# Performance work log

Measured on AMD Instinct MI355X. Metric: run time of the kernel, lower is better.

Reference implementation:

```python
import jax, jax.numpy as jnp
import numpy as np

B, V, C_IN, C_OUT = 4, 8, 32, 32
H, W = 256, 256
G = H * W
K_NEIGHBORS = 3


def compute_adjacency_tilde(extrinsics, k):
    Bv, Vv = extrinsics.shape[:2]
    R = extrinsics[:, :, :3, :3]
    t = extrinsics[:, :, :3, 3]
    # camera centers: -R^T t
    centers = -jnp.einsum('bvji,bvj->bvi', R, t)                 # (B,V,3)
    diff = centers[:, :, None, :] - centers[:, None, :, :]
    dist_sq = jnp.sum(diff * diff, axis=-1)                      # (B,V,V)
    eye = jnp.eye(Vv, dtype=bool)
    sim = jnp.where(eye, -jnp.inf, -dist_sq)
    A_overlap = 1.0 / (1.0 + jnp.sqrt(dist_sq + 1e-6))
    if 0 < k < Vv:
        _, topk_idx = jax.lax.top_k(sim, k)                      # (B,V,k)
        mask = jnp.sum(jax.nn.one_hot(topk_idx, Vv, dtype=jnp.float32), axis=-2) > 0
        A = A_overlap * mask.astype(A_overlap.dtype)
    else:
        A = A_overlap
    A = jnp.where(eye, 1.0, A)                                   # diagonal = 1
    deg = jnp.sum(A, axis=-1, keepdims=True)
    A_tilde = A / (deg + (deg == 0).astype(deg.dtype))
    return A, A_tilde


def setup_inputs() -> dict:
    key = jax.random.key(0)
    k1, k2, k3, k4, k5 = jax.random.split(key, 5)
    features = jax.random.normal(k1, (B, V, G, C_IN), dtype=jnp.float32)
    # projected pixel coords in [0, W-1] x [0, H-1]
    uv = jax.random.uniform(k2, (B, V, V, G, 2), dtype=jnp.float32)
    xy_coords = uv * jnp.array([W - 1, H - 1], dtype=jnp.float32)
    extrinsics = jax.random.normal(k3, (B, V, 4, 4), dtype=jnp.float32)
    W_lin = jax.random.normal(k4, (C_IN, C_OUT), dtype=jnp.float32) * 0.1
    b_lin = jax.random.normal(k5, (C_OUT,), dtype=jnp.float32) * 0.01
    return {"features": features, "xy_coords": xy_coords, "extrinsics": extrinsics,
            "W_lin": W_lin, "b_lin": b_lin}


def reference(features, xy_coords, extrinsics, W_lin, b_lin):
    feats = features @ W_lin + b_lin                              # (B,V,G,D)
    Bv, Vv, Gv, D = feats.shape
    HW = H * W
    A, A_tilde = compute_adjacency_tilde(extrinsics, K_NEIGHBORS)
    # flattened pixel indices per (batch, src view, tgt view, gaussian)
    x = jnp.clip(jnp.round(xy_coords[..., 0]), 0, W - 1).astype(jnp.int32)
    y = jnp.clip(jnp.round(xy_coords[..., 1]), 0, H - 1).astype(jnp.int32)
    idx = y * W + x                                               # (B,Vsrc,Vtgt,G)
    batch_off = jnp.arange(Bv, dtype=jnp.int32)[:, None] * HW
    outs = []
    for i in range(Vv):  # small fixed number of target views
        w_i = A_tilde[:, i][:, :, None, None]                     # (B,Vsrc,1,1)
        data = (feats * w_i).reshape(Bv * Vv * Gv, D)
        seg = (idx[:, :, i].reshape(Bv, Vv * Gv) + batch_off).reshape(-1)
        grid = jax.ops.segment_sum(data, seg, num_segments=Bv * HW)
        grid = grid.reshape(Bv, HW, D)                            # (B,HW,D)
        self_idx = idx[:, i, i]                                   # (B,G)
        outs.append(jnp.take_along_axis(grid, self_idx[..., None], axis=1))
    stacked = jnp.stack(outs, axis=1)                             # (B,V,G,D)
    return stacked, A
```

## Files before the change

kernel.cpp:

```cpp
#include <hip/hip_runtime.h>
#include <math.h>

#define NB 4
#define NV 8
#define NC 32
#define NG 65536
#define IMGW 256
#define NBI 32
#define RSPLIT 8
#define RBINS (NG / RSPLIT)
#define K4SPLIT 32
#define K4BINS (NG / K4SPLIT)
#define K4CAP 24576
#define CAP4A 1272
#define PART_STRIDE 19456
#define START_STRIDE 65544
#define SORT_STRIDE (1u << 20)
#define SENTINEL (8u << 27)

static constexpr long long STACKED_ELEMS = (long long)NB * NV * NG * NC;

typedef __attribute__((ext_vector_type(8))) short short8;
typedef __attribute__((ext_vector_type(4))) float f32x4;
typedef __attribute__((ext_vector_type(4))) unsigned int u32x4;
typedef __attribute__((ext_vector_type(4))) float f32x4c;

static constexpr size_t OFF_AT    = 0;
static constexpr size_t OFF_RTOT  = 1024;
static constexpr size_t OFF_GSC   = 3584;
static constexpr size_t OFF_START = 8192;
static constexpr size_t OFF_CNT   = OFF_START + (size_t)NBI * START_STRIDE * 4;
static constexpr size_t OFF_PIX   = OFF_CNT + (size_t)NBI * NG * 4;
static constexpr size_t OFF_SORT  = OFF_PIX + (size_t)NBI * NV * NG * 2;
static constexpr size_t OFF_FB16  = OFF_SORT + (size_t)NBI * SORT_STRIDE * 4;
static constexpr size_t OFF_PARTS = OFF_FB16;

__device__ __forceinline__ unsigned short f2bf(float f)
{
    unsigned int u = __float_as_uint(f);
    return (unsigned short)((u + 0x7FFFu + ((u >> 16) & 1u)) >> 16);
}

__global__ __launch_bounds__(256) void k1_pix(const float2* __restrict__ xy,
                                              unsigned short* __restrict__ pixarr,
                                              const float* __restrict__ ext,
                                              float* __restrict__ A_out,
                                              float* __restrict__ At_out)
{
    if (blockIdx.x == 16384) {
        __shared__ float ctr[NB * NV][3];
        __shared__ float Dsh[NB * NV * NV];
        int t = threadIdx.x;
        if (t < NB * NV) {
            const float* E = ext + t * 16;
            #pragma unroll
            for (int i = 0; i < 3; i++) {
                float s = E[0 * 4 + i] * E[0 * 4 + 3]
                        + E[1 * 4 + i] * E[1 * 4 + 3]
                        + E[2 * 4 + i] * E[2 * 4 + 3];
                ctr[t][i] = -s;
            }
        }
        __syncthreads();
        {
            int b = t >> 6, i = (t >> 3) & 7, j = t & 7;
            float dx = ctr[b * 8 + i][0] - ctr[b * 8 + j][0];
            float dy = ctr[b * 8 + i][1] - ctr[b * 8 + j][1];
            float dz = ctr[b * 8 + i][2] - ctr[b * 8 + j][2];
            Dsh[t] = dx * dx + dy * dy + dz * dz;
        }
        __syncthreads();
        if (t < NB * NV) {
            int ri = t & 7;
            const float* drow = &Dsh[t * 8];
            bool chosen[8] = {false, false, false, false, false, false, false, false};
            for (int n = 0; n < 3; n++) {
                int best = -1; float bs = -3.0e38f;
                for (int j2 = 0; j2 < 8; j2++) {
                    if (j2 == ri || chosen[j2]) continue;
                    float s = -drow[j2];
                    if (s > bs) { bs = s; best = j2; }
                }
                chosen[best] = true;
            }
            float row[8]; float deg = 0.f;
            #pragma unroll
            for (int j2 = 0; j2 < 8; j2++) {
                float a = 0.f;
                if (j2 == ri)        a = 1.0f;
                else if (chosen[j2]) a = 1.0f / (1.0f + sqrtf(drow[j2] + 1e-6f));
                row[j2] = a; deg += a;
            }
            float dn = deg + (deg == 0.f ? 1.f : 0.f);
            #pragma unroll
            for (int j2 = 0; j2 < 8; j2++) {
                A_out[t * 8 + j2]  = row[j2];
                At_out[t * 8 + j2] = row[j2] / dn;
            }
        }
        return;
    }
    unsigned int base = blockIdx.x * 1024 + threadIdx.x;
    #pragma unroll
    for (int k = 0; k < 4; k++) {
        unsigned int tid = base + k * 256;
        float2 p = xy[tid];
        float px = fminf(fmaxf(rintf(p.x), 0.f), (float)(IMGW - 1));
        float py = fminf(fmaxf(rintf(p.y), 0.f), (float)(IMGW - 1));
        unsigned int pix = (unsigned int)py * IMGW + (unsigned int)px;
        unsigned int g = tid & 0xFFFFu;
        unsigned int i = (tid >> 16) & 7u;
        unsigned int j = (tid >> 19) & 7u;
        unsigned int b = tid >> 22;
        unsigned int bi = (b << 3) | i;
        pixarr[(((bi << 3) | j) << 16) | g] = (unsigned short)pix;
    }
}

__global__ __launch_bounds__(1024) void k2_hist(const unsigned short* __restrict__ pixarr,
                                                unsigned int* __restrict__ cnt,
                                                unsigned int* __restrict__ rtot)
{
    __shared__ unsigned int hist[RBINS];
    int t = threadIdx.x;
    unsigned int bi = blockIdx.x & 31u;
    unsigned int r  = blockIdx.x >> 5;
    unsigned int r0 = r * RBINS;
    for (int k = t; k < RBINS; k += 1024) hist[k] = 0;
    __syncthreads();
    const uint4* src = (const uint4*)(pixarr + ((size_t)bi << 19));
    for (int it = 0; it < 8; it++) {
        uint4 vv[8];
        #pragma unroll
        for (int q = 0; q < 8; q++)
            vv[q] = src[t + (it * 8 + q) * 1024];
        #pragma unroll
        for (int q = 0; q < 8; q++) {
            const unsigned int* vw = (const unsigned int*)&vv[q];
            #pragma unroll
            for (int h = 0; h < 4; h++) {
                unsigned int w = vw[h];
                unsigned int p0 = (w & 0xFFFFu) - r0;
                unsigned int p1 = (w >> 16) - r0;
                if (p0 < RBINS) atomicAdd(&hist[p0], 1u);
                if (p1 < RBINS) atomicAdd(&hist[p1], 1u);
            }
        }
    }
    __syncthreads();
    unsigned int* dst = cnt + ((size_t)bi << 16) + r0;
    unsigned int psum = 0;
    for (int k = t; k < RBINS; k += 1024) {
        unsigned int v = hist[k];
        dst[k] = v;
        psum += (v + 7u) & ~7u;
    }
    __syncthreads();
    hist[t] = psum;
    __syncthreads();
    for (int off = 512; off; off >>= 1) {
        if (t < off) hist[t] += hist[t + off];
        __syncthreads();
    }
    if (t == 0) rtot[bi * 8 + r] = hist[0];
}

__global__ __launch_bounds__(1024) void k3c_scan(const unsigned int* __restrict__ cnt,
                                                 const unsigned int* __restrict__ rtot,
                                                 unsigned int* __restrict__ start)
{
    __shared__ unsigned int lc[RBINS];
    __shared__ unsigned int bs[1024];
    int t = threadIdx.x;
    unsigned int bi = blockIdx.x & 31u;
    unsigned int r  = blockIdx.x >> 5;
    unsigned int r0 = r * RBINS;
    unsigned int rb = 0, rtotal = 0;
    #pragma unroll
    for (int q = 0; q < 8; q++) {
        unsigned int v = rtot[bi * 8 + q];
        if ((unsigned int)q < r) rb += v;
        rtotal += v;
    }
    const unsigned int* c = cnt + ((size_t)bi << 16) + r0;
    #pragma unroll
    for (int q = 0; q < 8; q++)
        lc[q * 1024 + t] = (c[q * 1024 + t] + 7u) & ~7u;
    __syncthreads();
    unsigned int v[8]; unsigned int s = 0;
    #pragma unroll
    for (int k = 0; k < 8; k++) { v[k] = s; s += lc[t * 8 + k]; }
    bs[t] = s;
    __syncthreads();
    for (int off = 1; off < 1024; off <<= 1) {
        unsigned int u = (t >= off) ? bs[t - off] : 0u;
        __syncthreads();
        bs[t] += u;
        __syncthreads();
    }
    unsigned int base = rb + bs[t] - s;
    #pragma unroll
    for (int k = 0; k < 8; k++) lc[t * 8 + k] = base + v[k];
    __syncthreads();
    unsigned int* st_ = start + (size_t)bi * START_STRIDE + r0;
    #pragma unroll
    for (int q = 0; q < 8; q++)
        st_[q * 1024 + t] = lc[q * 1024 + t];
    if (r == 7 && t == 0)
        start[(size_t)bi * START_STRIDE + NG] = rtotal;
}

__global__ __launch_bounds__(1024) void k4a_part(const unsigned short* __restrict__ pixarr,
                                                 unsigned int* __restrict__ gsc,
                                                 unsigned int* __restrict__ parts)
{
    extern __shared__ unsigned int dynA[];
    unsigned int* cur32 = dynA;
    unsigned int* res   = dynA + 32;
    unsigned int* lcnt  = dynA + 64;
    unsigned int* lbuck = dynA + 96;
    int t = threadIdx.x;
    unsigned int bi    = blockIdx.x & 31u;
    unsigned int chunk = blockIdx.x >> 5;
    if (t < 32) cur32[t] = 0;
    __syncthreads();
    const uint4* src = (const uint4*)(pixarr + ((size_t)bi << 19)) + (chunk << 12);
    unsigned int idx0 = chunk << 15;
    #pragma unroll
    for (int it = 0; it < 4; it++) {
        uint4 v = src[t + it * 1024];
        unsigned int base_idx = idx0 + (t + it * 1024) * 8;
        const unsigned int* vw = (const unsigned int*)&v;
        #pragma unroll
        for (int h = 0; h < 8; h++) {
            unsigned int pix = (h & 1) ? (vw[h >> 1] >> 16) : (vw[h >> 1] & 0xFFFFu);
            unsigned int sub = pix >> 11;
            unsigned int pv = ((pix & 0x7FFu) << 19) | (base_idx + h);
            unsigned int slot = atomicAdd(&cur32[sub], 1u);
            if (slot < CAP4A) {
                lbuck[sub * CAP4A + slot] = pv;
            } else {
                unsigned int gs = atomicAdd(&gsc[(bi << 5) | sub], 1u);
                parts[(size_t)((bi << 5) | sub) * PART_STRIDE + gs] = pv;
            }
        }
    }
    __syncthreads();
    if (t < 32) {
        unsigned int n = cur32[t];
        n = n < CAP4A ? n : CAP4A;
        lcnt[t] = n;
        res[t] = atomicAdd(&gsc[(bi << 5) | t], n);
    }
    __syncthreads();
    for (int s = 0; s < 32; s++) {
        unsigned int n = lcnt[s];
        unsigned int b0 = res[s];
        unsigned int* dst = parts + (size_t)((bi << 5) | s) * PART_STRIDE + b0;
        const unsigned int* sb = lbuck + s * CAP4A;
        for (unsigned int k = t; k < n; k += 1024) dst[k] = sb[k];
    }
}

__global__ __launch_bounds__(1024) void k4b_fill(const unsigned int* __restrict__ gsc,
                                                 const unsigned int* __restrict__ parts,
                                                 const unsigned int* __restrict__ start,
                                                 unsigned int* __restrict__ sorted)
{
    extern __shared__ unsigned int dynB[];
    unsigned int* cur = dynB;
    unsigned int* buf = dynB + K4BINS;
    int t = threadIdx.x;
    unsigned int bi  = blockIdx.x & 31u;
    unsigned int sub = blockIdx.x >> 5;
    unsigned int bin0 = sub * K4BINS;
    const unsigned int* stg = start + (size_t)bi * START_STRIDE;
    unsigned int base = stg[bin0];
    unsigned int end  = stg[bin0 + K4BINS];
    unsigned int size = end - base;
    unsigned int n = gsc[(bi << 5) | sub];
    const unsigned int* seg = parts + (size_t)((bi << 5) | sub) * PART_STRIDE;
    unsigned int* dstbase = sorted + (size_t)bi * SORT_STRIDE;

    if (size <= K4CAP) {
        #pragma unroll 2
        for (int k = t; k < K4BINS; k += 1024) cur[k] = stg[bin0 + k] - base;
        for (int k = t; k < (int)size; k += 1024) buf[k] = SENTINEL;
        __syncthreads();
        for (unsigned int k = t; k < n; k += 1024) {
            unsigned int pv = seg[k];
            unsigned int bin = pv >> 19;
            unsigned int slot = atomicAdd(&cur[bin], 1u);
            buf[slot] = (((pv >> 16) & 7u) << 27) | ((pv & 0x7FFFFu) << 6);
        }
        __syncthreads();
        uint4* gdst = (uint4*)(dstbase + base);
        const uint4* lsrc = (const uint4*)buf;
        int n4 = (int)(size >> 2);
        for (int k = t; k < n4; k += 1024) gdst[k] = lsrc[k];
    } else {
        #pragma unroll 2
        for (int k = t; k < K4BINS; k += 1024) cur[k] = stg[bin0 + k];
        __syncthreads();
        for (unsigned int k = t; k < n; k += 1024) {
            unsigned int pv = seg[k];
            unsigned int bin = pv >> 19;
            unsigned int slot = atomicAdd(&cur[bin], 1u);
            dstbase[slot] = (((pv >> 16) & 7u) << 27) | ((pv & 0x7FFFFu) << 6);
        }
        __syncthreads();
        for (int k = t; k < K4BINS; k += 1024) {
            unsigned int e = stg[bin0 + k + 1];
            for (unsigned int x = cur[k]; x < e; x++) dstbase[x] = SENTINEL;
        }
    }
}

__global__ __launch_bounds__(256) void kf_conv(const float* __restrict__ src,
                                               ushort4* __restrict__ dst)
{
    unsigned int base = blockIdx.x * 1024 + threadIdx.x;
    #pragma unroll
    for (int k = 0; k < 4; k++) {
        unsigned int idx = base + k * 256;
        f32x4c v = __builtin_nontemporal_load((const f32x4c*)(src) + idx);
        ushort4 o;
        o.x = f2bf(v.x); o.y = f2bf(v.y); o.z = f2bf(v.z); o.w = f2bf(v.w);
        dst[idx] = o;
    }
}

__global__ __launch_bounds__(256, 4) void b_gather(
    const unsigned short* __restrict__ fb16,
    const unsigned short* __restrict__ pixarr,
    const unsigned int* __restrict__ start,
    const unsigned int* __restrict__ sorted,
    const float* __restrict__ Wlin,
    const float* __restrict__ blin,
    const float* __restrict__ At,
    float* __restrict__ out,
    int b)
{
    __shared__ float At9[NBI][16];
    int t = threadIdx.x;
    int c4 = t & 7;
    int grp = t >> 3;

    unsigned int bidx = blockIdx.x;
    unsigned int i  = bidx & 7u;
    unsigned int gc = bidx >> 3;
    unsigned int bi = ((unsigned int)b << 3) | i;
    unsigned int g0 = gc << 5;
    unsigned int g = g0 + grp;

    unsigned int pix = pixarr[(((bi << 3) | i) << 16) | g];
    const unsigned int* st = start + (size_t)bi * START_STRIDE;
    unsigned int s0 = st[pix];
    unsigned int e0 = st[pix + 1];
    const unsigned int* pl = sorted + (size_t)bi * SORT_STRIDE;
    u32x4 pa = __builtin_nontemporal_load((const u32x4*)(pl + s0));
    u32x4 pb = __builtin_nontemporal_load((const u32x4*)(pl + s0 + 4));

    At9[t >> 3][t & 7] = At[t];
    At9[t >> 3][8 + (t & 7)] = 0.f;
    int l = t & 63;
    short8 bf0, bf1;
    #pragma unroll
    for (int j = 0; j < 8; j++) {
        int kk = (l >> 4) * 8 + j;
        bf0[j] = (short)f2bf(Wlin[kk * NC + (l & 15)]);
        bf1[j] = (short)f2bf(Wlin[kk * NC + 16 + (l & 15)]);
    }
    const char* fbB = (const char*)fb16;
    unsigned int cb = c4 << 3;
    __syncthreads();

    const float* Atrow = At9[bi];
    float ax = 0.f, ay = 0.f, az = 0.f, aw = 0.f, wsum = 0.f;
    for (unsigned int k0 = s0; k0 < e0; k0 += 8) {
        unsigned int pv[8] = {pa.x, pa.y, pa.z, pa.w, pb.x, pb.y, pb.z, pb.w};
        uint2 uv[8];
        #pragma unroll
        for (int h = 0; h < 8; h++)
            uv[h] = *(const uint2*)(fbB + ((pv[h] & 0x01FFFFC0u) | cb));
        if (k0 + 8 < e0) {
            pa = __builtin_nontemporal_load((const u32x4*)(pl + k0 + 8));
            pb = __builtin_nontemporal_load((const u32x4*)(pl + k0 + 12));
        }
        float wv[8];
        #pragma unroll
        for (int h = 0; h < 8; h++)
            wv[h] = Atrow[pv[h] >> 27];
        #pragma unroll
        for (int h = 0; h < 8; h++) {
            ax = fmaf(wv[h], __uint_as_float(uv[h].x << 16), ax);
            ay = fmaf(wv[h], __uint_as_float(uv[h].x & 0xFFFF0000u), ay);
            az = fmaf(wv[h], __uint_as_float(uv[h].y << 16), az);
            aw = fmaf(wv[h], __uint_as_float(uv[h].y & 0xFFFF0000u), aw);
            wsum += wv[h];
        }
    }

    int r = l & 15;
    int kb = l >> 4;
    int s0l = (((r & 7) << 3) | (kb << 1)) & 63;
    int s1l = s0l | 1;
    float v0x = __shfl(ax, s0l, 64), v0y = __shfl(ay, s0l, 64);
    float v0z = __shfl(az, s0l, 64), v0w = __shfl(aw, s0l, 64);
    float v1x = __shfl(ax, s1l, 64), v1y = __shfl(ay, s1l, 64);
    float v1z = __shfl(az, s1l, 64), v1w = __shfl(aw, s1l, 64);
    short8 af;
    if (r < 8) {
        af[0] = (short)f2bf(v0x); af[1] = (short)f2bf(v0y);
        af[2] = (short)f2bf(v0z); af[3] = (short)f2bf(v0w);
        af[4] = (short)f2bf(v1x); af[5] = (short)f2bf(v1y);
        af[6] = (short)f2bf(v1z); af[7] = (short)f2bf(v1w);
    } else {
        af = short8{0, 0, 0, 0, 0, 0, 0, 0};
    }
    float bias0 = blin[l & 15];
    float bias1 = blin[16 + (l & 15)];
    f32x4 c0, c1;
    #pragma unroll
    for (int q = 0; q < 4; q++) {
        int row = kb * 4 + q;
        float wvx = __shfl(wsum, (row << 3) & 63, 64);
        wvx = (row < 8) ? wvx : 0.f;
        c0[q] = bias0 * wvx;
        c1[q] = bias1 * wvx;
    }
    c0 = __builtin_amdgcn_mfma_f32_16x16x32_bf16(af, bf0, c0, 0, 0, 0);
    c1 = __builtin_amdgcn_mfma_f32_16x16x32_bf16(af, bf1, c1, 0, 0, 0);
    if (l < 32) {
        size_t rowbase = (((size_t)bi << 16) | g0) + (t >> 6) * 8;
        #pragma unroll
        for (int q = 0; q < 4; q++) {
            size_t rr = rowbase + (l >> 4) * 4 + q;
            __builtin_nontemporal_store(c0[q], &out[rr * NC + (l & 15)]);
            __builtin_nontemporal_store(c1[q], &out[rr * NC + 16 + (l & 15)]);
        }
    }
}

extern "C" void kernel_launch(void* const* d_in, const int* in_sizes, int n_in,
                              void* d_out, int out_size, void* d_ws, size_t ws_size,
                              hipStream_t stream)
{
    const float* features = (const float*)d_in[0];
    const float* xy       = (const float*)d_in[1];
    const float* ext      = (const float*)d_in[2];
    const float* Wlin     = (const float*)d_in[3];
    const float* blin     = (const float*)d_in[4];
    float* out = (float*)d_out;

    char* ws = (char*)d_ws;
    float*          At     = (float*)(ws + OFF_AT);
    unsigned int*   rtot   = (unsigned int*)(ws + OFF_RTOT);
    unsigned int*   gsc    = (unsigned int*)(ws + OFF_GSC);
    unsigned int*   start  = (unsigned int*)(ws + OFF_START);
    unsigned int*   cnt    = (unsigned int*)(ws + OFF_CNT);
    unsigned short* pixarr = (unsigned short*)(ws + OFF_PIX);
    unsigned int*   sorted = (unsigned int*)(ws + OFF_SORT);
    unsigned int*   parts  = (unsigned int*)(ws + OFF_PARTS);
    unsigned short* fb16   = (unsigned short*)(ws + OFF_FB16);

    static const size_t k4a_lds = (96 + 32 * CAP4A) * sizeof(unsigned int);
    static const size_t k4b_lds = (K4BINS + K4CAP) * sizeof(unsigned int);
    hipFuncSetAttribute((const void*)k4a_part,
                        hipFuncAttributeMaxDynamicSharedMemorySize, (int)k4a_lds);
    hipFuncSetAttribute((const void*)k4b_fill,
                        hipFuncAttributeMaxDynamicSharedMemorySize, (int)k4b_lds);

    k1_pix<<<16385, 256, 0, stream>>>((const float2*)xy, pixarr, ext,
                                      out + STACKED_ELEMS, At);
    k2_hist<<<NBI * RSPLIT, 1024, 0, stream>>>(pixarr, cnt, rtot);
    k3c_scan<<<NBI * RSPLIT, 1024, 0, stream>>>(cnt, rtot, start);

    hipMemsetAsync(gsc, 0, 1024 * sizeof(unsigned int), stream);
    k4a_part<<<NBI * 16, 1024, k4a_lds, stream>>>(pixarr, gsc, parts);
    k4b_fill<<<NBI * K4SPLIT, 1024, k4b_lds, stream>>>(gsc, parts, start, sorted);

    for (int b = 0; b < NB; b++) {
        const float* src = features + (((size_t)b) << 19) * NC;
        kf_conv<<<4096, 256, 0, stream>>>(src, (ushort4*)fb16);
        b_gather<<<16384, 256, 0, stream>>>(fb16, pixarr, start, sorted,
                                            Wlin, blin, At, out, b);
    }
}
```

Before: 592.1 us.

## Derive bin offsets from partitioned buckets instead of a full histogram pass

Drops the separate histogram and scan kernels that each re-read the whole pixel-index array. Per-bucket histograms and local prefix sums are now computed from the already partitioned bucket data, followed by a tiny cross-bucket scan. The fill kernel writes the global start offsets itself. This removes one full pass over the pixel array, at the cost of two extra small launches and a per-bucket local-start buffer.

```diff
diff --git a/kernel.cpp b/kernel.cpp
--- a/kernel.cpp
+++ b/kernel.cpp
@@ -7,8 +7,6 @@
 #define NG 65536
 #define IMGW 256
 #define NBI 32
-#define RSPLIT 8
-#define RBINS (NG / RSPLIT)
 #define K4SPLIT 32
 #define K4BINS (NG / K4SPLIT)
 #define K4CAP 24576
@@ -25,15 +23,16 @@
 typedef __attribute__((ext_vector_type(4))) unsigned int u32x4;
 typedef __attribute__((ext_vector_type(4))) float f32x4c;
 
-static constexpr size_t OFF_AT    = 0;
-static constexpr size_t OFF_RTOT  = 1024;
-static constexpr size_t OFF_GSC   = 3584;
-static constexpr size_t OFF_START = 8192;
-static constexpr size_t OFF_CNT   = OFF_START + (size_t)NBI * START_STRIDE * 4;
-static constexpr size_t OFF_PIX   = OFF_CNT + (size_t)NBI * NG * 4;
-static constexpr size_t OFF_SORT  = OFF_PIX + (size_t)NBI * NV * NG * 2;
-static constexpr size_t OFF_FB16  = OFF_SORT + (size_t)NBI * SORT_STRIDE * 4;
-static constexpr size_t OFF_PARTS = OFF_FB16;
+static constexpr size_t OFF_AT     = 0;
+static constexpr size_t OFF_PTOT   = 1024;
+static constexpr size_t OFF_PBASE  = 5120;
+static constexpr size_t OFF_GSC    = 9216;
+static constexpr size_t OFF_START  = 16384;
+static constexpr size_t OFF_LSTART = OFF_START + (size_t)NBI * START_STRIDE * 4;
+static constexpr size_t OFF_PIX    = OFF_LSTART + (size_t)1024 * K4BINS * 4;
+static constexpr size_t OFF_SORT   = OFF_PIX + (size_t)NBI * NV * NG * 2;
+static constexpr size_t OFF_FB16   = OFF_SORT + (size_t)NBI * SORT_STRIDE * 4;
+static constexpr size_t OFF_PARTS  = OFF_FB16;
 
 __device__ __forceinline__ unsigned short f2bf(float f)
 {
@@ -117,99 +116,6 @@
     }
 }
 
-__global__ __launch_bounds__(1024) void k2_hist(const unsigned short* __restrict__ pixarr,
-                                                unsigned int* __restrict__ cnt,
-                                                unsigned int* __restrict__ rtot)
-{
-    __shared__ unsigned int hist[RBINS];
-    int t = threadIdx.x;
-    unsigned int bi = blockIdx.x & 31u;
-    unsigned int r  = blockIdx.x >> 5;
-    unsigned int r0 = r * RBINS;
-    for (int k = t; k < RBINS; k += 1024) hist[k] = 0;
-    __syncthreads();
-    const uint4* src = (const uint4*)(pixarr + ((size_t)bi << 19));
-    for (int it = 0; it < 8; it++) {
-        uint4 vv[8];
-        #pragma unroll
-        for (int q = 0; q < 8; q++)
-            vv[q] = src[t + (it * 8 + q) * 1024];
-        #pragma unroll
-        for (int q = 0; q < 8; q++) {
-            const unsigned int* vw = (const unsigned int*)&vv[q];
-            #pragma unroll
-            for (int h = 0; h < 4; h++) {
-                unsigned int w = vw[h];
-                unsigned int p0 = (w & 0xFFFFu) - r0;
-                unsigned int p1 = (w >> 16) - r0;
-                if (p0 < RBINS) atomicAdd(&hist[p0], 1u);
-                if (p1 < RBINS) atomicAdd(&hist[p1], 1u);
-            }
-        }
-    }
-    __syncthreads();
-    unsigned int* dst = cnt + ((size_t)bi << 16) + r0;
-    unsigned int psum = 0;
-    for (int k = t; k < RBINS; k += 1024) {
-        unsigned int v = hist[k];
-        dst[k] = v;
-        psum += (v + 7u) & ~7u;
-    }
-    __syncthreads();
-    hist[t] = psum;
-    __syncthreads();
-    for (int off = 512; off; off >>= 1) {
-        if (t < off) hist[t] += hist[t + off];
-        __syncthreads();
-    }
-    if (t == 0) rtot[bi * 8 + r] = hist[0];
-}
-
-__global__ __launch_bounds__(1024) void k3c_scan(const unsigned int* __restrict__ cnt,
-                                                 const unsigned int* __restrict__ rtot,
-                                                 unsigned int* __restrict__ start)
-{
-    __shared__ unsigned int lc[RBINS];
-    __shared__ unsigned int bs[1024];
-    int t = threadIdx.x;
-    unsigned int bi = blockIdx.x & 31u;
-    unsigned int r  = blockIdx.x >> 5;
-    unsigned int r0 = r * RBINS;
-    unsigned int rb = 0, rtotal = 0;
-    #pragma unroll
-    for (int q = 0; q < 8; q++) {
-        unsigned int v = rtot[bi * 8 + q];
-        if ((unsigned int)q < r) rb += v;
-        rtotal += v;
-    }
-    const unsigned int* c = cnt + ((size_t)bi << 16) + r0;
-    #pragma unroll
-    for (int q = 0; q < 8; q++)
-        lc[q * 1024 + t] = (c[q * 1024 + t] + 7u) & ~7u;
-    __syncthreads();
-    unsigned int v[8]; unsigned int s = 0;
-    #pragma unroll
-    for (int k = 0; k < 8; k++) { v[k] = s; s += lc[t * 8 + k]; }
-    bs[t] = s;
-    __syncthreads();
-    for (int off = 1; off < 1024; off <<= 1) {
-        unsigned int u = (t >= off) ? bs[t - off] : 0u;
-        __syncthreads();
-        bs[t] += u;
-        __syncthreads();
-    }
-    unsigned int base = rb + bs[t] - s;
-    #pragma unroll
-    for (int k = 0; k < 8; k++) lc[t * 8 + k] = base + v[k];
-    __syncthreads();
-    unsigned int* st_ = start + (size_t)bi * START_STRIDE + r0;
-    #pragma unroll
-    for (int q = 0; q < 8; q++)
-        st_[q * 1024 + t] = lc[q * 1024 + t];
-    if (r == 7 && t == 0)
-        start[(size_t)bi * START_STRIDE + NG] = rtotal;
-}
-
 __global__ __launch_bounds__(1024) void k4a_part(const unsigned short* __restrict__ pixarr,
                                                  unsigned int* __restrict__ gsc,
                                                  unsigned int* __restrict__ parts)
@@ -262,10 +168,67 @@
     }
 }
 
-__global__ __launch_bounds__(1024) void k4b_fill(const unsigned int* __restrict__ gsc,
+__global__ __launch_bounds__(1024) void k4h_hist(const unsigned int* __restrict__ gsc,
                                                  const unsigned int* __restrict__ parts,
-                                                 const unsigned int* __restrict__ start,
-                                                 unsigned int* __restrict__ sorted)
+                                                 unsigned int* __restrict__ lstart,
+                                                 unsigned int* __restrict__ ptot)
+{
+    __shared__ unsigned int hist[K4BINS];
+    __shared__ unsigned int bs[1024];
+    int t = threadIdx.x;
+    unsigned int bi  = blockIdx.x & 31u;
+    unsigned int sub = blockIdx.x >> 5;
+    unsigned int n = gsc[(bi << 5) | sub];
+    const unsigned int* seg = parts + (size_t)((bi << 5) | sub) * PART_STRIDE;
+    hist[t] = 0; hist[t + 1024] = 0;
+    __syncthreads();
+    for (unsigned int k = t; k < n; k += 1024)
+        atomicAdd(&hist[seg[k] >> 19], 1u);
+    __syncthreads();
+    unsigned int c0 = (hist[2 * t] + 7u) & ~7u;
+    unsigned int c1 = (hist[2 * t + 1] + 7u) & ~7u;
+    unsigned int s = c0 + c1;
+    bs[t] = s;
+    __syncthreads();
+    for (int off = 1; off < 1024; off <<= 1) {
+        unsigned int u = (t >= off) ? bs[t - off] : 0u;
+        __syncthreads();
+        bs[t] += u;
+        __syncthreads();
+    }
+    unsigned int base = bs[t] - s;
+    __syncthreads();
+    hist[2 * t] = base;
+    hist[2 * t + 1] = base + c0;
+    __syncthreads();
+    unsigned int* ls = lstart + (size_t)blockIdx.x * K4BINS;
+    ls[t] = hist[t]; ls[t + 1024] = hist[t + 1024];
+    if (t == 1023) ptot[blockIdx.x] = bs[1023];
+}
+
+__global__ __launch_bounds__(64) void k4s_scan(const unsigned int* __restrict__ ptot,
+                                               unsigned int* __restrict__ pbase,
+                                               unsigned int* __restrict__ start)
+{
+    int t = threadIdx.x;
+    if (t < 32) {
+        unsigned int run = 0;
+        #pragma unroll
+        for (int q = 0; q < 32; q++) {
+            pbase[(q << 5) | t] = run;
+            run += ptot[(q << 5) | t];
+        }
+        start[(size_t)t * START_STRIDE + NG] = run;
+    }
+}
+
+__global__ __launch_bounds__(1024) void k4c_fill(const unsigned int* __restrict__ gsc,
+                                                 const unsigned int* __restrict__ parts,
+                                                 const unsigned int* __restrict__ lstart,
+                                                 const unsigned int* __restrict__ pbase,
+                                                 const unsigned int* __restrict__ ptot,
+                                                 unsigned int* __restrict__ sorted,
+                                                 unsigned int* __restrict__ start)
 {
     extern __shared__ unsigned int dynB[];
     unsigned int* cur = dynB;
@@ -273,18 +236,22 @@
     int t = threadIdx.x;
     unsigned int bi  = blockIdx.x & 31u;
     unsigned int sub = blockIdx.x >> 5;
-    unsigned int bin0 = sub * K4BINS;
-    const unsigned int* stg = start + (size_t)bi * START_STRIDE;
-    unsigned int base = stg[bin0];
-    unsigned int end  = stg[bin0 + K4BINS];
-    unsigned int size = end - base;
     unsigned int n = gsc[(bi << 5) | sub];
+    unsigned int base = pbase[(sub << 5) | bi];
+    unsigned int size = ptot[(sub << 5) | bi];
+    const unsigned int* ls = lstart + (size_t)((sub << 5) | bi) * K4BINS;
     const unsigned int* seg = parts + (size_t)((bi << 5) | sub) * PART_STRIDE;
     unsigned int* dstbase = sorted + (size_t)bi * SORT_STRIDE;
+    unsigned int* stw = start + (size_t)bi * START_STRIDE + sub * K4BINS;
+
+    #pragma unroll 2
+    for (int k = t; k < K4BINS; k += 1024) {
+        unsigned int v = ls[k];
+        stw[k] = base + v;
+        cur[k] = v;
+    }
 
     if (size <= K4CAP) {
-        #pragma unroll 2
-        for (int k = t; k < K4BINS; k += 1024) cur[k] = stg[bin0 + k] - base;
         for (int k = t; k < (int)size; k += 1024) buf[k] = SENTINEL;
         __syncthreads();
         for (unsigned int k = t; k < n; k += 1024) {
@@ -299,19 +266,17 @@
         int n4 = (int)(size >> 2);
         for (int k = t; k < n4; k += 1024) gdst[k] = lsrc[k];
     } else {
-        #pragma unroll 2
-        for (int k = t; k < K4BINS; k += 1024) cur[k] = stg[bin0 + k];
         __syncthreads();
         for (unsigned int k = t; k < n; k += 1024) {
             unsigned int pv = seg[k];
             unsigned int bin = pv >> 19;
             unsigned int slot = atomicAdd(&cur[bin], 1u);
-            dstbase[slot] = (((pv >> 16) & 7u) << 27) | ((pv & 0x7FFFFu) << 6);
+            dstbase[base + slot] = (((pv >> 16) & 7u) << 27) | ((pv & 0x7FFFFu) << 6);
         }
         __syncthreads();
         for (int k = t; k < K4BINS; k += 1024) {
-            unsigned int e = stg[bin0 + k + 1];
-            for (unsigned int x = cur[k]; x < e; x++) dstbase[x] = SENTINEL;
+            unsigned int e = (k < K4BINS - 1) ? ls[k + 1] : size;
+            for (unsigned int x = cur[k]; x < e; x++) dstbase[base + x] = SENTINEL;
         }
     }
 }
@@ -455,30 +420,32 @@
 
     char* ws = (char*)d_ws;
     float*          At     = (float*)(ws + OFF_AT);
-    unsigned int*   rtot   = (unsigned int*)(ws + OFF_RTOT);
+    unsigned int*   ptot   = (unsigned int*)(ws + OFF_PTOT);
+    unsigned int*   pbase  = (unsigned int*)(ws + OFF_PBASE);
     unsigned int*   gsc    = (unsigned int*)(ws + OFF_GSC);
     unsigned int*   start  = (unsigned int*)(ws + OFF_START);
-    unsigned int*   cnt    = (unsigned int*)(ws + OFF_CNT);
+    unsigned int*   lstart = (unsigned int*)(ws + OFF_LSTART);
     unsigned short* pixarr = (unsigned short*)(ws + OFF_PIX);
     unsigned int*   sorted = (unsigned int*)(ws + OFF_SORT);
     unsigned int*   parts  = (unsigned int*)(ws + OFF_PARTS);
     unsigned short* fb16   = (unsigned short*)(ws + OFF_FB16);
 
     static const size_t k4a_lds = (96 + 32 * CAP4A) * sizeof(unsigned int);
-    static const size_t k4b_lds = (K4BINS + K4CAP) * sizeof(unsigned int);
+    static const size_t k4c_lds = (K4BINS + K4CAP) * sizeof(unsigned int);
     hipFuncSetAttribute((const void*)k4a_part,
                         hipFuncAttributeMaxDynamicSharedMemorySize, (int)k4a_lds);
-    hipFuncSetAttribute((const void*)k4b_fill,
-                        hipFuncAttributeMaxDynamicSharedMemorySize, (int)k4b_lds);
+    hipFuncSetAttribute((const void*)k4c_fill,
+                        hipFuncAttributeMaxDynamicSharedMemorySize, (int)k4c_lds);
 
     k1_pix<<<16385, 256, 0, stream>>>((const float2*)xy, pixarr, ext,
                                       out + STACKED_ELEMS, At);
-    k2_hist<<<NBI * RSPLIT, 1024, 0, stream>>>(pixarr, cnt, rtot);
-    k3c_scan<<<NBI * RSPLIT, 1024, 0, stream>>>(cnt, rtot, start);
 
     hipMemsetAsync(gsc, 0, 1024 * sizeof(unsigned int), stream);
     k4a_part<<<NBI * 16, 1024, k4a_lds, stream>>>(pixarr, gsc, parts);
-    k4b_fill<<<NBI * K4SPLIT, 1024, k4b_lds, stream>>>(gsc, parts, start, sorted);
+    k4h_hist<<<1024, 1024, 0, stream>>>(gsc, parts, lstart, ptot);
+    k4s_scan<<<1, 64, 0, stream>>>(ptot, pbase, start);
+    k4c_fill<<<1024, 1024, k4c_lds, stream>>>(gsc, parts, lstart, pbase, ptot,
+                                              sorted, start);
 
     for (int b = 0; b < NB; b++) {
         const float* src = features + (((size_t)b) << 19) * NC;
```

Result: no change. 580.5 us (-2.0%).
